# Kernel tuning notes

Hardware: AMD Instinct MI355X
Metric: run time of the kernel (lower is better)

Reference implementation:

```python
import jax, jax.numpy as jnp
import numpy as np

IN_SIZE = 4096   # input_size
OUT_SIZE = 4096  # output_size
RANK = 1024      # len(S_4), multiple of 32
GROUPSIZE = 128
BITS = 4
PACK = 32 // BITS  # 8 nibbles per int32
MAXQ_MASK = (1 << BITS) - 1  # 15


def _dequant4(qweight, qzeros, scales, g_idx):
    """GPTQ 4-bit dequant. qweight: int32 [K//8, N]; qzeros: int32 [G, N//8];
    scales: [G, N]; g_idx: int32 [K]. Returns W [K, N] with
    W[k, n] = (int4[k, n] - (zero4[g_idx[k], n] + 1)) * scales[g_idx[k], n]."""
    shifts = (jnp.arange(PACK, dtype=jnp.int32) * BITS)
    K = qweight.shape[0] * PACK
    N = qweight.shape[1]
    # unpack along rows: [K//8, 8, N] -> [K, N]
    intw = ((qweight[:, None, :] >> shifts[None, :, None]) & MAXQ_MASK).reshape(K, N)
    # unpack along cols: [G, N//8, 8] -> [G, N]; pack() stored zeros-1, so add 1 back
    zeros = ((qzeros[:, :, None] >> shifts[None, None, :]) & MAXQ_MASK).reshape(qzeros.shape[0], N) + 1
    sc = scales[g_idx]            # [K, N]
    zr = zeros[g_idx].astype(scales.dtype)  # [K, N]
    return (intw.astype(scales.dtype) - zr) * sc


def setup_inputs() -> dict:
    key = jax.random.key(0)
    ks = jax.random.split(key, 9)
    qweight_V = jax.random.randint(ks[0], (IN_SIZE // PACK, RANK), 0, 2**31 - 1, dtype=jnp.int32)
    qzeros_V = jax.random.randint(ks[1], (IN_SIZE // GROUPSIZE, RANK // PACK), 0, 2**31 - 1, dtype=jnp.int32)
    scales_V = jax.random.uniform(ks[2], (IN_SIZE // GROUPSIZE, RANK), dtype=jnp.float32) * 0.01 + 1e-3
    g_idx_V = (jnp.arange(IN_SIZE, dtype=jnp.int32) // GROUPSIZE).astype(jnp.int32)
    qweight_U = jax.random.randint(ks[3], (RANK // PACK, OUT_SIZE), 0, 2**31 - 1, dtype=jnp.int32)
    qzeros_U = jax.random.randint(ks[4], (RANK // GROUPSIZE, OUT_SIZE // PACK), 0, 2**31 - 1, dtype=jnp.int32)
    scales_U = jax.random.uniform(ks[5], (RANK // GROUPSIZE, OUT_SIZE), dtype=jnp.float32) * 0.01 + 1e-3
    g_idx_U = (jnp.arange(RANK, dtype=jnp.int32) // GROUPSIZE).astype(jnp.int32)
    S = jax.random.uniform(ks[6], (RANK,), dtype=jnp.float32) + 0.1  # singular values
    x = jax.random.normal(ks[7], (4, 2048, IN_SIZE), dtype=jnp.float32)
    return {"x": x,
            "qweight_V": qweight_V, "qzeros_V": qzeros_V, "scales_V": scales_V, "g_idx_V": g_idx_V,
            "qweight_U": qweight_U, "qzeros_U": qzeros_U, "scales_U": scales_U, "g_idx_U": g_idx_U,
            "S": S}


def reference(x, qweight_V, qzeros_V, scales_V, g_idx_V,
              qweight_U, qzeros_U, scales_U, g_idx_U, S):
    # weight_V: dequantized [IN_SIZE, RANK]; weight_U: dequantized [RANK, OUT_SIZE]
    weight_V = _dequant4(qweight_V, qzeros_V, scales_V, g_idx_V)
    weight_U = _dequant4(qweight_U, qzeros_U, scales_U, g_idx_U)
    # forward returns (weight_V @ diag(S) @ weight_U).T  -> [OUT_SIZE, IN_SIZE]
    # (the x @ W_V @ diag(S) @ W_U activation path in the source is dead code
    #  w.r.t. the returned value)
    return ((weight_V * S[None, :]) @ weight_U).T
```

## Files before the change

kernel.cpp:

```cpp
#include <hip/hip_runtime.h>

typedef __attribute__((ext_vector_type(8))) short bf16x8;
typedef __attribute__((ext_vector_type(4))) float f32x4;

__device__ __forceinline__ short f2bf(float f) {
  unsigned u = __builtin_bit_cast(unsigned, f);
  u += 0x7fffu + ((u >> 16) & 1u);
  return (short)(u >> 16);
}


__global__ __launch_bounds__(256) void dequant_fused(
    const int* __restrict__ qw_V, const int* __restrict__ qz_V,
    const float* __restrict__ sc_V, const float* __restrict__ S,
    short* __restrict__ A,
    const int* __restrict__ qw_U, const int* __restrict__ qz_U,
    const float* __restrict__ sc_U, short* __restrict__ B) {
  const int bid = blockIdx.x;
  if (bid < 2048) {
    const int t    = bid * 256 + threadIdx.x;
    const int tile = t >> 11;
    const int blk  = (t >> 6) & 31;
    const int lane = t & 63;
    const int panel = tile >> 4, kt = tile & 15;
    const int m  = (panel << 8) + (((blk >> 4) & 1) << 7) + (((blk >> 1) & 7) << 4) + (lane & 15);
    const int r0 = (kt << 6) + ((blk & 1) << 5) + ((lane >> 4) << 3);
    const int g  = m >> 7;
    const int sh = (m & 7) << 2;
    const int zw = qz_V[(g << 7) + (r0 >> 3)];
    const int*   wq  = qw_V + (m >> 3) * 1024 + r0;
    const float* scp = sc_V + (g << 10) + r0;
    const float* sp  = S + r0;
    bf16x8 res;
#pragma unroll
    for (int e = 0; e < 8; ++e) {
      int q = (wq[e] >> sh) & 15;
      int z = ((zw >> (e << 2)) & 15) + 1;
      res[e] = f2bf((float)(q - z) * scp[e] * sp[e]);
    }
    *(bf16x8*)(A + ((size_t)t << 3)) = res;
  } else {
    const int t    = (bid - 2048) * 256 + threadIdx.x;
    const int tile = t >> 11;
    const int blk  = (t >> 6) & 31;
    const int lane = t & 63;
    const int panel = tile >> 4, kt = tile & 15;
    const int n  = (panel << 8) + (((blk >> 3) & 3) << 6) + (((blk >> 1) & 3) << 4) + (lane & 15);
    const int r0 = (kt << 6) + ((blk & 1) << 5) + ((lane >> 4) << 3);
    const int w  = qw_U[(r0 >> 3) * 4096 + n];
    const int g  = r0 >> 7;
    const int zw = qz_U[(g << 9) + (n >> 3)];
    const int z  = ((zw >> ((n & 7) << 2)) & 15) + 1;
    const float s = sc_U[(g << 12) + n];
    bf16x8 res;
#pragma unroll
    for (int e = 0; e < 8; ++e) {
      int q = (w >> (e << 2)) & 15;
      res[e] = f2bf((float)(q - z) * s);
    }
    *(bf16x8*)(B + ((size_t)t << 3)) = res;
  }
}

#define GLL(g, l)                                                              \
  __builtin_amdgcn_global_load_lds(                                            \
      (const __attribute__((address_space(1))) void*)(g),                      \
      (__attribute__((address_space(3))) void*)(l), 16, 0, 0)

__global__ __launch_bounds__(512, 2) void gemm256(const short* __restrict__ A,
                                                  const short* __restrict__ B,
                                                  float* __restrict__ out) {
  __shared__ __align__(16) char lds[131072];
  const int tid  = threadIdx.x;
  const int lane = tid & 63;
  const int wid  = tid >> 6;
  const int wm   = wid >> 2;
  const int wn   = wid & 3;
  const int bid = ((blockIdx.x & 7) << 5) | (blockIdx.x >> 3);
  const int mp = bid >> 4;
  const int np = bid & 15;

  const short* gA = A + ((size_t)(mp * 16) << 14) + (wid << 11) + (lane << 3);
  const short* gB = B + ((size_t)(np * 16) << 14) + (wid << 11) + (lane << 3);

#define STGA(buf, ktv) do {                                                    \
    const short* s_ = gA + ((ktv) << 14);                                      \
    char* d_ = lds + (buf) + (wid << 12);                                      \
    GLL(s_,        d_);                                                        \
    GLL(s_ +  512, d_ + 1024);                                                 \
    GLL(s_ + 1024, d_ + 2048);                                                 \
    GLL(s_ + 1536, d_ + 3072);                                                 \
  } while (0)
#define STGB(buf, ktv) do {                                                    \
    const short* s_ = gB + ((ktv) << 14);                                      \
    char* d_ = lds + (buf) + 32768 + (wid << 12);                              \
    GLL(s_,        d_);                                                        \
    GLL(s_ +  512, d_ + 1024);                                                 \
    GLL(s_ + 1024, d_ + 2048);                                                 \
    GLL(s_ + 1536, d_ + 3072);                                                 \
  } while (0)

  const char* Ard = lds + (wm << 14) + (lane << 4);
  const char* Brd = lds + 32768 + (wn << 13) + (lane << 4);

  f32x4 acc[8][4];
#pragma unroll
  for (int mi = 0; mi < 8; ++mi)
#pragma unroll
    for (int ni = 0; ni < 4; ++ni) acc[mi][ni] = f32x4{0.f, 0.f, 0.f, 0.f};

  bf16x8 alo[4][2], ahi[4][2], bh0[2][2], bh1[2][2];

  STGB(0, 0);
  STGA(0, 0);
  STGB(65536, 1);
  STGA(65536, 1);
  asm volatile("s_waitcnt vmcnt(8)" ::: "memory");
  __builtin_amdgcn_s_barrier();

  for (int kt = 0; kt < 16; ++kt) {
    const int curbuf = (kt & 1) << 16;

#pragma unroll
    for (int i = 0; i < 4; ++i) {
      alo[i][0] = *(const bf16x8*)(Ard + curbuf + (i << 11));
      alo[i][1] = *(const bf16x8*)(Ard + curbuf + (i << 11) + 1024);
    }
#pragma unroll
    for (int j = 0; j < 2; ++j) {
      bh0[j][0] = *(const bf16x8*)(Brd + curbuf + (j << 11));
      bh0[j][1] = *(const bf16x8*)(Brd + curbuf + (j << 11) + 1024);
    }
#pragma unroll
    for (int j = 0; j < 2; ++j) {
      bh1[j][0] = *(const bf16x8*)(Brd + curbuf + 4096 + (j << 11));
      bh1[j][1] = *(const bf16x8*)(Brd + curbuf + 4096 + (j << 11) + 1024);
    }
    asm volatile("s_waitcnt lgkmcnt(4)" ::: "memory");
    __builtin_amdgcn_sched_barrier(0);
    __builtin_amdgcn_s_setprio(1);
#pragma unroll
    for (int kk = 0; kk < 2; ++kk)
#pragma unroll
      for (int i = 0; i < 4; ++i)
#pragma unroll
        for (int j = 0; j < 2; ++j)
          acc[i][j] = __builtin_amdgcn_mfma_f32_16x16x32_bf16(
              alo[i][kk], bh0[j][kk], acc[i][j], 0, 0, 0);
    __builtin_amdgcn_s_setprio(0);

#pragma unroll
    for (int i = 0; i < 4; ++i) {
      ahi[i][0] = *(const bf16x8*)(Ard + curbuf + 8192 + (i << 11));
      ahi[i][1] = *(const bf16x8*)(Ard + curbuf + 8192 + (i << 11) + 1024);
    }
    asm volatile("s_waitcnt lgkmcnt(8)" ::: "memory");
    __builtin_amdgcn_sched_barrier(0);
    __builtin_amdgcn_s_setprio(1);
#pragma unroll
    for (int kk = 0; kk < 2; ++kk)
#pragma unroll
      for (int i = 0; i < 4; ++i)
#pragma unroll
        for (int j = 0; j < 2; ++j)
          acc[i][2 + j] = __builtin_amdgcn_mfma_f32_16x16x32_bf16(
              alo[i][kk], bh1[j][kk], acc[i][2 + j], 0, 0, 0);
    __builtin_amdgcn_s_setprio(0);
    __builtin_amdgcn_s_barrier();

    if (kt < 14) STGB(curbuf, kt + 2);
    asm volatile("s_waitcnt lgkmcnt(0)" ::: "memory");
    __builtin_amdgcn_sched_barrier(0);
    __builtin_amdgcn_s_setprio(1);
#pragma unroll
    for (int kk = 0; kk < 2; ++kk)
#pragma unroll
      for (int i = 0; i < 4; ++i)
#pragma unroll
        for (int j = 0; j < 2; ++j)
          acc[4 + i][2 + j] = __builtin_amdgcn_mfma_f32_16x16x32_bf16(
              ahi[i][kk], bh1[j][kk], acc[4 + i][2 + j], 0, 0, 0);
    __builtin_amdgcn_s_setprio(0);
    __builtin_amdgcn_s_barrier();

    if (kt < 14) STGA(curbuf, kt + 2);
    __builtin_amdgcn_s_setprio(1);
#pragma unroll
    for (int kk = 0; kk < 2; ++kk)
#pragma unroll
      for (int i = 0; i < 4; ++i)
#pragma unroll
        for (int j = 0; j < 2; ++j)
          acc[4 + i][j] = __builtin_amdgcn_mfma_f32_16x16x32_bf16(
              ahi[i][kk], bh0[j][kk], acc[4 + i][j], 0, 0, 0);
    __builtin_amdgcn_s_setprio(0);
    if (kt == 14) asm volatile("s_waitcnt vmcnt(0)" ::: "memory");
    else          asm volatile("s_waitcnt vmcnt(8)" ::: "memory");
    __builtin_amdgcn_s_barrier();
  }

  const int mbase = (mp << 8) + (wm << 7) + ((lane >> 4) << 2);
  const int nbase = (np << 8) + (wn << 6) + (lane & 15);
#pragma unroll
  for (int mi = 0; mi < 8; ++mi)
#pragma unroll
    for (int ni = 0; ni < 4; ++ni)
      *(f32x4*)(out + (size_t)(nbase + ni * 16) * 4096 + mbase + mi * 16) =
          acc[mi][ni];
#undef STGA
#undef STGB
}

extern "C" void kernel_launch(void* const* d_in, const int* in_sizes, int n_in,
                              void* d_out, int out_size, void* d_ws, size_t ws_size,
                              hipStream_t stream) {
  const int*   qw_V = (const int*)d_in[1];
  const int*   qz_V = (const int*)d_in[2];
  const float* sc_V = (const float*)d_in[3];
  const int*   qw_U = (const int*)d_in[5];
  const int*   qz_U = (const int*)d_in[6];
  const float* sc_U = (const float*)d_in[7];
  const float* S    = (const float*)d_in[9];

  short* A = (short*)d_ws;
  short* B = (short*)d_ws + 4096 * 1024;
  float* out = (float*)d_out;

  dequant_fused<<<4096, 256, 0, stream>>>(qw_V, qz_V, sc_V, S, A,
                                          qw_U, qz_U, sc_U, B);
  gemm256<<<256, 512, 0, stream>>>(A, B, out);
}
```

Before: 51.68 us.

## Restructure GEMM main loop into half-tile LDS buffers with finer-grained prefetch

The GEMM mainloop is rewritten to split each K-tile's A and B into halves held in separate LDS regions. Global-to-LDS loads are issued at a finer granularity, interleaved between the four MFMA clusters, and the loop is unrolled by two tiles so buffer addresses are compile-time. The aim is to spread memory traffic more evenly across compute phases and keep the MFMA pipe fed. In exchange it adds more barriers per tile, which could increase synchronization overhead.

```diff
diff --git a/kernel.cpp b/kernel.cpp
--- a/kernel.cpp
+++ b/kernel.cpp
@@ -80,28 +80,29 @@
   const int mp = bid >> 4;
   const int np = bid & 15;
 
-  const short* gA = A + ((size_t)(mp * 16) << 14) + (wid << 11) + (lane << 3);
-  const short* gB = B + ((size_t)(np * 16) << 14) + (wid << 11) + (lane << 3);
-
-#define STGA(buf, ktv) do {                                                    \
-    const short* s_ = gA + ((ktv) << 14);                                      \
-    char* d_ = lds + (buf) + (wid << 12);                                      \
-    GLL(s_,        d_);                                                        \
-    GLL(s_ +  512, d_ + 1024);                                                 \
-    GLL(s_ + 1024, d_ + 2048);                                                 \
-    GLL(s_ + 1536, d_ + 3072);                                                 \
+  const short* gAp = A + (size_t)mp * 262144 + tid * 8;
+  const short* gBp = B + (size_t)np * 262144 + tid * 8;
+  const int wofs = wid << 10;
+
+#define STGA_H(tile, half) do {                                                \
+    const short* s_ = gAp + (tile) * 16384 + (half) * 8192;                    \
+    char* d_ = lds + ((((tile) & 1) * 2 + (half)) << 14) + wofs;               \
+    GLL(s_, d_);                                                               \
+    GLL(s_ + 4096, d_ + 8192);                                                 \
   } while (0)
-#define STGB(buf, ktv) do {                                                    \
-    const short* s_ = gB + ((ktv) << 14);                                      \
-    char* d_ = lds + (buf) + 32768 + (wid << 12);                              \
-    GLL(s_,        d_);                                                        \
-    GLL(s_ +  512, d_ + 1024);                                                 \
-    GLL(s_ + 1024, d_ + 2048);                                                 \
-    GLL(s_ + 1536, d_ + 3072);                                                 \
+#define STGB_H(tile, half) do {                                                \
+    const short* s_ = gBp + (tile) * 16384 + (half) * 8192;                    \
+    char* d_ = lds + 65536 + ((((tile) & 1) * 2 + (half)) << 14) + wofs;       \
+    GLL(s_, d_);                                                               \
+    GLL(s_ + 4096, d_ + 8192);                                                 \
   } while (0)
 
-  const char* Ard = lds + (wm << 14) + (lane << 4);
-  const char* Brd = lds + 32768 + (wn << 13) + (lane << 4);
+  const char* aB[2];
+  const char* bB[2];
+  aB[0] = lds + (wm << 14) + (lane << 4);
+  aB[1] = lds + ((2 + wm) << 14) + (lane << 4);
+  bB[0] = lds + 65536 + ((wn >> 1) << 14) + ((wn & 1) << 13) + (lane << 4);
+  bB[1] = lds + 65536 + (((wn >> 1) + 2) << 14) + ((wn & 1) << 13) + (lane << 4);
 
   f32x4 acc[8][4];
 #pragma unroll
@@ -111,92 +112,90 @@
 
   bf16x8 alo[4][2], ahi[4][2], bh0[2][2], bh1[2][2];
 
-  STGB(0, 0);
-  STGA(0, 0);
-  STGB(65536, 1);
-  STGA(65536, 1);
-  asm volatile("s_waitcnt vmcnt(8)" ::: "memory");
-  __builtin_amdgcn_s_barrier();
-
-  for (int kt = 0; kt < 16; ++kt) {
-    const int curbuf = (kt & 1) << 16;
-
-#pragma unroll
-    for (int i = 0; i < 4; ++i) {
-      alo[i][0] = *(const bf16x8*)(Ard + curbuf + (i << 11));
-      alo[i][1] = *(const bf16x8*)(Ard + curbuf + (i << 11) + 1024);
-    }
-#pragma unroll
-    for (int j = 0; j < 2; ++j) {
-      bh0[j][0] = *(const bf16x8*)(Brd + curbuf + (j << 11));
-      bh0[j][1] = *(const bf16x8*)(Brd + curbuf + (j << 11) + 1024);
-    }
-#pragma unroll
-    for (int j = 0; j < 2; ++j) {
-      bh1[j][0] = *(const bf16x8*)(Brd + curbuf + 4096 + (j << 11));
-      bh1[j][1] = *(const bf16x8*)(Brd + curbuf + 4096 + (j << 11) + 1024);
-    }
-    asm volatile("s_waitcnt lgkmcnt(4)" ::: "memory");
-    __builtin_amdgcn_sched_barrier(0);
-    __builtin_amdgcn_s_setprio(1);
-#pragma unroll
-    for (int kk = 0; kk < 2; ++kk)
-#pragma unroll
-      for (int i = 0; i < 4; ++i)
-#pragma unroll
-        for (int j = 0; j < 2; ++j)
-          acc[i][j] = __builtin_amdgcn_mfma_f32_16x16x32_bf16(
-              alo[i][kk], bh0[j][kk], acc[i][j], 0, 0, 0);
-    __builtin_amdgcn_s_setprio(0);
-
-#pragma unroll
-    for (int i = 0; i < 4; ++i) {
-      ahi[i][0] = *(const bf16x8*)(Ard + curbuf + 8192 + (i << 11));
-      ahi[i][1] = *(const bf16x8*)(Ard + curbuf + 8192 + (i << 11) + 1024);
-    }
-    asm volatile("s_waitcnt lgkmcnt(8)" ::: "memory");
-    __builtin_amdgcn_sched_barrier(0);
-    __builtin_amdgcn_s_setprio(1);
-#pragma unroll
-    for (int kk = 0; kk < 2; ++kk)
-#pragma unroll
-      for (int i = 0; i < 4; ++i)
-#pragma unroll
-        for (int j = 0; j < 2; ++j)
-          acc[i][2 + j] = __builtin_amdgcn_mfma_f32_16x16x32_bf16(
-              alo[i][kk], bh1[j][kk], acc[i][2 + j], 0, 0, 0);
-    __builtin_amdgcn_s_setprio(0);
-    __builtin_amdgcn_s_barrier();
-
-    if (kt < 14) STGB(curbuf, kt + 2);
-    asm volatile("s_waitcnt lgkmcnt(0)" ::: "memory");
-    __builtin_amdgcn_sched_barrier(0);
-    __builtin_amdgcn_s_setprio(1);
-#pragma unroll
-    for (int kk = 0; kk < 2; ++kk)
-#pragma unroll
-      for (int i = 0; i < 4; ++i)
-#pragma unroll
-        for (int j = 0; j < 2; ++j)
-          acc[4 + i][2 + j] = __builtin_amdgcn_mfma_f32_16x16x32_bf16(
-              ahi[i][kk], bh1[j][kk], acc[4 + i][2 + j], 0, 0, 0);
-    __builtin_amdgcn_s_setprio(0);
-    __builtin_amdgcn_s_barrier();
-
-    if (kt < 14) STGA(curbuf, kt + 2);
-    __builtin_amdgcn_s_setprio(1);
-#pragma unroll
-    for (int kk = 0; kk < 2; ++kk)
-#pragma unroll
-      for (int i = 0; i < 4; ++i)
-#pragma unroll
-        for (int j = 0; j < 2; ++j)
-          acc[4 + i][j] = __builtin_amdgcn_mfma_f32_16x16x32_bf16(
-              ahi[i][kk], bh0[j][kk], acc[4 + i][j], 0, 0, 0);
-    __builtin_amdgcn_s_setprio(0);
-    if (kt == 14) asm volatile("s_waitcnt vmcnt(0)" ::: "memory");
-    else          asm volatile("s_waitcnt vmcnt(8)" ::: "memory");
-    __builtin_amdgcn_s_barrier();
+#define CL16(AF, BF, MI0, NJ0)                                                 \
+  _Pragma("unroll")                                                            \
+  for (int kk = 0; kk < 2; ++kk)                                               \
+    _Pragma("unroll")                                                          \
+    for (int i = 0; i < 4; ++i)                                                \
+      _Pragma("unroll")                                                        \
+      for (int j = 0; j < 2; ++j)                                              \
+        acc[(MI0) + i][(NJ0) + j] = __builtin_amdgcn_mfma_f32_16x16x32_bf16(   \
+            AF[i][kk], BF[j][kk], acc[(MI0) + i][(NJ0) + j], 0, 0, 0);
+
+#define RD_ALO(ab) _Pragma("unroll") for (int i = 0; i < 4; ++i) {             \
+    alo[i][0] = *(const bf16x8*)((ab) + (i * 2) * 1024);                       \
+    alo[i][1] = *(const bf16x8*)((ab) + (i * 2 + 1) * 1024); }
+#define RD_AHI(ab) _Pragma("unroll") for (int i = 0; i < 4; ++i) {             \
+    ahi[i][0] = *(const bf16x8*)((ab) + ((i + 4) * 2) * 1024);                 \
+    ahi[i][1] = *(const bf16x8*)((ab) + ((i + 4) * 2 + 1) * 1024); }
+#define RD_B0(bb) _Pragma("unroll") for (int j = 0; j < 2; ++j) {              \
+    bh0[j][0] = *(const bf16x8*)((bb) + (j * 2) * 1024);                       \
+    bh0[j][1] = *(const bf16x8*)((bb) + (j * 2 + 1) * 1024); }
+#define RD_B1(bb) _Pragma("unroll") for (int j = 0; j < 2; ++j) {              \
+    bh1[j][0] = *(const bf16x8*)((bb) + ((j + 2) * 2) * 1024);                 \
+    bh1[j][1] = *(const bf16x8*)((bb) + ((j + 2) * 2 + 1) * 1024); }
+
+#define WLG0  asm volatile("s_waitcnt lgkmcnt(0)" ::: "memory");               \
+              __builtin_amdgcn_sched_barrier(0)
+#define BAR   __builtin_amdgcn_s_barrier()
+#define PRIO1 __builtin_amdgcn_s_setprio(1)
+#define PRIO0 __builtin_amdgcn_s_setprio(0)
+
+  STGA_H(0, 0); STGA_H(0, 1); STGB_H(0, 0); STGB_H(0, 1);
+  STGB_H(1, 0); STGB_H(1, 1);
+  asm volatile("s_waitcnt vmcnt(4)" ::: "memory");
+  BAR;
+
+  for (int it = 0; it < 8; ++it) {
+    const int t0 = it << 1;
+    const int last = (it == 7);
+    const char* a0 = aB[0];
+    const char* b0 = bB[0];
+    const char* a1 = aB[1];
+    const char* b1 = bB[1];
+
+    RD_ALO(a0); RD_B0(b0);
+    STGA_H(t0 + 1, 0);
+    BAR; WLG0;
+    PRIO1; CL16(alo, bh0, 0, 0); PRIO0;
+    BAR;
+    RD_B1(b0);
+    STGA_H(t0 + 1, 1);
+    BAR; WLG0;
+    PRIO1; CL16(alo, bh1, 0, 2); PRIO0;
+    BAR;
+    RD_AHI(a0);
+    if (!last) STGB_H(t0 + 2, 0);
+    BAR; WLG0;
+    PRIO1; CL16(ahi, bh1, 4, 2); PRIO0;
+    BAR;
+    if (!last) STGB_H(t0 + 2, 1);
+    BAR;
+    PRIO1; CL16(ahi, bh0, 4, 0); PRIO0;
+    if (last) asm volatile("s_waitcnt vmcnt(0)" ::: "memory");
+    else      asm volatile("s_waitcnt vmcnt(4)" ::: "memory");
+    BAR;
+
+    RD_ALO(a1); RD_B0(b1);
+    if (!last) STGA_H(t0 + 2, 0);
+    BAR; WLG0;
+    PRIO1; CL16(alo, bh0, 0, 0); PRIO0;
+    BAR;
+    RD_B1(b1);
+    if (!last) STGA_H(t0 + 2, 1);
+    BAR; WLG0;
+    PRIO1; CL16(alo, bh1, 0, 2); PRIO0;
+    BAR;
+    RD_AHI(a1);
+    if (!last) STGB_H(t0 + 3, 0);
+    BAR; WLG0;
+    PRIO1; CL16(ahi, bh1, 4, 2); PRIO0;
+    BAR;
+    if (!last) STGB_H(t0 + 3, 1);
+    BAR;
+    PRIO1; CL16(ahi, bh0, 4, 0); PRIO0;
+    if (!last) asm volatile("s_waitcnt vmcnt(4)" ::: "memory");
+    BAR;
   }
 
   const int mbase = (mp << 8) + (wm << 7) + ((lane >> 4) << 2);
@@ -207,8 +206,17 @@
     for (int ni = 0; ni < 4; ++ni)
       *(f32x4*)(out + (size_t)(nbase + ni * 16) * 4096 + mbase + mi * 16) =
           acc[mi][ni];
-#undef STGA
-#undef STGB
+#undef STGA_H
+#undef STGB_H
+#undef CL16
+#undef RD_ALO
+#undef RD_AHI
+#undef RD_B0
+#undef RD_B1
+#undef WLG0
+#undef BAR
+#undef PRIO1
+#undef PRIO0
 }
 
 extern "C" void kernel_launch(void* const* d_in, const int* in_sizes, int n_in,
```

Measured after the change: 52.39 us. Within noise of the previous version (+1.4%).

## Switch GEMM to 128x256 tiles with 32-wide K steps and matching pre-tiled layout

Applied to the files above, without the earlier changes.

Replaces the 256x256 GEMM tile (K-step 64, 128KB LDS, 2 blocks/CU) with a 128x256 tile using K-step 32, 48KB LDS and a simpler one-shot LDS read followed by 16 MFMAs per iteration. It launches 512 blocks instead of 256 to fill all CUs on the MI355X, and the dequant kernels now write A and B in the new pre-tiled layout. The cost is less reuse per tile and twice as many barrier-separated iterations. The per-iteration schedule also loses the interleaving of LDS reads with MFMAs.

```diff
diff --git a/kernel.cpp b/kernel.cpp
--- a/kernel.cpp
+++ b/kernel.cpp
@@ -19,12 +19,11 @@
   const int bid = blockIdx.x;
   if (bid < 2048) {
     const int t    = bid * 256 + threadIdx.x;
-    const int tile = t >> 11;
-    const int blk  = (t >> 6) & 31;
+    const int tile = t >> 9;
+    const int blk  = (t >> 6) & 7;
     const int lane = t & 63;
-    const int panel = tile >> 4, kt = tile & 15;
-    const int m  = (panel << 8) + (((blk >> 4) & 1) << 7) + (((blk >> 1) & 7) << 4) + (lane & 15);
-    const int r0 = (kt << 6) + ((blk & 1) << 5) + ((lane >> 4) << 3);
+    const int m  = (tile >> 5) * 128 + blk * 16 + (lane & 15);
+    const int r0 = (tile & 31) * 32 + ((lane >> 4) << 3);
     const int g  = m >> 7;
     const int sh = (m & 7) << 2;
     const int zw = qz_V[(g << 7) + (r0 >> 3)];
@@ -41,12 +40,11 @@
     *(bf16x8*)(A + ((size_t)t << 3)) = res;
   } else {
     const int t    = (bid - 2048) * 256 + threadIdx.x;
-    const int tile = t >> 11;
-    const int blk  = (t >> 6) & 31;
+    const int tile = t >> 10;
+    const int blk  = (t >> 6) & 15;
     const int lane = t & 63;
-    const int panel = tile >> 4, kt = tile & 15;
-    const int n  = (panel << 8) + (((blk >> 3) & 3) << 6) + (((blk >> 1) & 3) << 4) + (lane & 15);
-    const int r0 = (kt << 6) + ((blk & 1) << 5) + ((lane >> 4) << 3);
+    const int n  = (tile >> 5) * 256 + blk * 16 + (lane & 15);
+    const int r0 = (tile & 31) * 32 + ((lane >> 4) << 3);
     const int w  = qw_U[(r0 >> 3) * 4096 + n];
     const int g  = r0 >> 7;
     const int zw = qz_U[(g << 9) + (n >> 3)];
@@ -67,148 +65,81 @@
       (const __attribute__((address_space(1))) void*)(g),                      \
       (__attribute__((address_space(3))) void*)(l), 16, 0, 0)
 
-__global__ __launch_bounds__(512, 2) void gemm256(const short* __restrict__ A,
-                                                  const short* __restrict__ B,
-                                                  float* __restrict__ out) {
-  __shared__ __align__(16) char lds[131072];
+__global__ __launch_bounds__(512, 4) void gemm128x256(
+    const short* __restrict__ A, const short* __restrict__ B,
+    float* __restrict__ out) {
+  __shared__ __align__(16) char lds[49152];
   const int tid  = threadIdx.x;
   const int lane = tid & 63;
   const int wid  = tid >> 6;
   const int wm   = wid >> 2;
   const int wn   = wid & 3;
-  const int bid = ((blockIdx.x & 7) << 5) | (blockIdx.x >> 3);
+  const int bid = ((blockIdx.x & 7) << 6) | (blockIdx.x >> 3);
   const int mp = bid >> 4;
   const int np = bid & 15;
 
-  const short* gA = A + ((size_t)(mp * 16) << 14) + (wid << 11) + (lane << 3);
-  const short* gB = B + ((size_t)(np * 16) << 14) + (wid << 11) + (lane << 3);
+  const short* gA = A + (size_t)mp * 32768 + tid * 8;
+  const short* gAp = A + (size_t)(mp * 32) * 4096 + tid * 8;
+  const short* gBp = B + (size_t)(np * 32) * 8192 + tid * 8;
+  char* const ldsA = lds + (wid << 10);
+  char* const ldsB = lds + 8192 + (wid << 10);
 
-#define STGA(buf, ktv) do {                                                    \
-    const short* s_ = gA + ((ktv) << 14);                                      \
-    char* d_ = lds + (buf) + (wid << 12);                                      \
-    GLL(s_,        d_);                                                        \
-    GLL(s_ +  512, d_ + 1024);                                                 \
-    GLL(s_ + 1024, d_ + 2048);                                                 \
-    GLL(s_ + 1536, d_ + 3072);                                                 \
-  } while (0)
-#define STGB(buf, ktv) do {                                                    \
-    const short* s_ = gB + ((ktv) << 14);                                      \
-    char* d_ = lds + (buf) + 32768 + (wid << 12);                              \
-    GLL(s_,        d_);                                                        \
-    GLL(s_ +  512, d_ + 1024);                                                 \
-    GLL(s_ + 1024, d_ + 2048);                                                 \
-    GLL(s_ + 1536, d_ + 3072);                                                 \
+#define STAGE(kt) do {                                                         \
+    const int bo_ = ((kt) & 1) * 24576;                                        \
+    GLL(gAp + (size_t)(kt) * 4096, ldsA + bo_);                                \
+    GLL(gBp + (size_t)(kt) * 8192, ldsB + bo_);                                \
+    GLL(gBp + (size_t)(kt) * 8192 + 4096, ldsB + bo_ + 8192);                  \
   } while (0)
 
-  const char* Ard = lds + (wm << 14) + (lane << 4);
-  const char* Brd = lds + 32768 + (wn << 13) + (lane << 4);
+  const char* Ard = lds + (lane << 4);
+  const char* Brd = lds + 8192 + (lane << 4);
 
-  f32x4 acc[8][4];
+  f32x4 acc[4][4];
 #pragma unroll
-  for (int mi = 0; mi < 8; ++mi)
+  for (int i = 0; i < 4; ++i)
 #pragma unroll
-    for (int ni = 0; ni < 4; ++ni) acc[mi][ni] = f32x4{0.f, 0.f, 0.f, 0.f};
+    for (int j = 0; j < 4; ++j) acc[i][j] = f32x4{0.f, 0.f, 0.f, 0.f};
 
-  bf16x8 alo[4][2], ahi[4][2], bh0[2][2], bh1[2][2];
-
-  STGB(0, 0);
-  STGA(0, 0);
-  STGB(65536, 1);
-  STGA(65536, 1);
-  asm volatile("s_waitcnt vmcnt(8)" ::: "memory");
+  STAGE(0);
+  STAGE(1);
+  asm volatile("s_waitcnt vmcnt(3)" ::: "memory");
   __builtin_amdgcn_s_barrier();
 
-  for (int kt = 0; kt < 16; ++kt) {
-    const int curbuf = (kt & 1) << 16;
-
+  for (int kt = 0; kt < 32; ++kt) {
+    const int bo = (kt & 1) * 24576;
+    bf16x8 a[4], b[4];
 #pragma unroll
-    for (int i = 0; i < 4; ++i) {
-      alo[i][0] = *(const bf16x8*)(Ard + curbuf + (i << 11));
-      alo[i][1] = *(const bf16x8*)(Ard + curbuf + (i << 11) + 1024);
-    }
+    for (int i = 0; i < 4; ++i)
+      a[i] = *(const bf16x8*)(Ard + bo + ((wm << 2) + i) * 1024);
 #pragma unroll
-    for (int j = 0; j < 2; ++j) {
-      bh0[j][0] = *(const bf16x8*)(Brd + curbuf + (j << 11));
-      bh0[j][1] = *(const bf16x8*)(Brd + curbuf + (j << 11) + 1024);
-    }
-#pragma unroll
-    for (int j = 0; j < 2; ++j) {
-      bh1[j][0] = *(const bf16x8*)(Brd + curbuf + 4096 + (j << 11));
-      bh1[j][1] = *(const bf16x8*)(Brd + curbuf + 4096 + (j << 11) + 1024);
-    }
-    asm volatile("s_waitcnt lgkmcnt(4)" ::: "memory");
+    for (int j = 0; j < 4; ++j)
+      b[j] = *(const bf16x8*)(Brd + bo + ((wn << 2) + j) * 1024);
+    asm volatile("s_waitcnt lgkmcnt(0)" ::: "memory");
     __builtin_amdgcn_sched_barrier(0);
+    __builtin_amdgcn_s_barrier();
+    if (kt < 30) STAGE(kt + 2);
     __builtin_amdgcn_s_setprio(1);
 #pragma unroll
-    for (int kk = 0; kk < 2; ++kk)
+    for (int i = 0; i < 4; ++i)
 #pragma unroll
-      for (int i = 0; i < 4; ++i)
-#pragma unroll
-        for (int j = 0; j < 2; ++j)
-          acc[i][j] = __builtin_amdgcn_mfma_f32_16x16x32_bf16(
-              alo[i][kk], bh0[j][kk], acc[i][j], 0, 0, 0);
+      for (int j = 0; j < 4; ++j)
+        acc[i][j] = __builtin_amdgcn_mfma_f32_16x16x32_bf16(
+            a[i], b[j], acc[i][j], 0, 0, 0);
     __builtin_amdgcn_s_setprio(0);
-
-#pragma unroll
-    for (int i = 0; i < 4; ++i) {
-      ahi[i][0] = *(const bf16x8*)(Ard + curbuf + 8192 + (i << 11));
-      ahi[i][1] = *(const bf16x8*)(Ard + curbuf + 8192 + (i << 11) + 1024);
-    }
-    asm volatile("s_waitcnt lgkmcnt(8)" ::: "memory");
-    __builtin_amdgcn_sched_barrier(0);
-    __builtin_amdgcn_s_setprio(1);
-#pragma unroll
-    for (int kk = 0; kk < 2; ++kk)
-#pragma unroll
-      for (int i = 0; i < 4; ++i)
-#pragma unroll
-        for (int j = 0; j < 2; ++j)
-          acc[i][2 + j] = __builtin_amdgcn_mfma_f32_16x16x32_bf16(
-              alo[i][kk], bh1[j][kk], acc[i][2 + j], 0, 0, 0);
-    __builtin_amdgcn_s_setprio(0);
-    __builtin_amdgcn_s_barrier();
-
-    if (kt < 14) STGB(curbuf, kt + 2);
-    asm volatile("s_waitcnt lgkmcnt(0)" ::: "memory");
-    __builtin_amdgcn_sched_barrier(0);
-    __builtin_amdgcn_s_setprio(1);
-#pragma unroll
-    for (int kk = 0; kk < 2; ++kk)
-#pragma unroll
-      for (int i = 0; i < 4; ++i)
-#pragma unroll
-        for (int j = 0; j < 2; ++j)
-          acc[4 + i][2 + j] = __builtin_amdgcn_mfma_f32_16x16x32_bf16(
-              ahi[i][kk], bh1[j][kk], acc[4 + i][2 + j], 0, 0, 0);
-    __builtin_amdgcn_s_setprio(0);
-    __builtin_amdgcn_s_barrier();
-
-    if (kt < 14) STGA(curbuf, kt + 2);
-    __builtin_amdgcn_s_setprio(1);
-#pragma unroll
-    for (int kk = 0; kk < 2; ++kk)
-#pragma unroll
-      for (int i = 0; i < 4; ++i)
-#pragma unroll
-        for (int j = 0; j < 2; ++j)
-          acc[4 + i][j] = __builtin_amdgcn_mfma_f32_16x16x32_bf16(
-              ahi[i][kk], bh0[j][kk], acc[4 + i][j], 0, 0, 0);
-    __builtin_amdgcn_s_setprio(0);
-    if (kt == 14) asm volatile("s_waitcnt vmcnt(0)" ::: "memory");
-    else          asm volatile("s_waitcnt vmcnt(8)" ::: "memory");
-    __builtin_amdgcn_s_barrier();
+    if (kt < 30)       asm volatile("s_waitcnt vmcnt(3)" ::: "memory");
+    else if (kt == 30) asm volatile("s_waitcnt vmcnt(0)" ::: "memory");
+    if (kt < 31) __builtin_amdgcn_s_barrier();
   }
 
-  const int mbase = (mp << 8) + (wm << 7) + ((lane >> 4) << 2);
+  const int mbase = (mp << 7) + (wm << 6) + ((lane >> 4) << 2);
   const int nbase = (np << 8) + (wn << 6) + (lane & 15);
 #pragma unroll
-  for (int mi = 0; mi < 8; ++mi)
+  for (int mi = 0; mi < 4; ++mi)
 #pragma unroll
     for (int ni = 0; ni < 4; ++ni)
       *(f32x4*)(out + (size_t)(nbase + ni * 16) * 4096 + mbase + mi * 16) =
           acc[mi][ni];
-#undef STGA
-#undef STGB
+#undef STAGE
 }
 
 extern "C" void kernel_launch(void* const* d_in, const int* in_sizes, int n_in,
@@ -228,5 +159,5 @@
 
   dequant_fused<<<4096, 256, 0, stream>>>(qw_V, qz_V, sc_V, S, A,
                                           qw_U, qz_U, sc_U, B);
-  gemm256<<<256, 512, 0, stream>>>(A, B, out);
+  gemm128x256<<<512, 512, 0, stream>>>(A, B, out);
 }
```

Measured after the change: 50.74 us. No clear change (-1.8%).
